# Kernel tuning notes

Measured on AMD Instinct MI355X. Metric: run time of the kernel, lower is better.

The kernel has to match this reference:

```python
import jax, jax.numpy as jnp
import numpy as np

B, NQ, NA, C, L = 8, 2048, 64, 128, 4  # batches, queries/mol, atoms/mol, hidden, num_layers
CUTOFF = 8.0
E_AQ, E_QQ = 131072, 262144


def _ln(x, g, b):
    m = x.mean(-1, keepdims=True)
    v = ((x - m) ** 2).mean(-1, keepdims=True)
    return (x - m) * jax.lax.rsqrt(v + 1e-5) * g + b


def _egnn(p, h_src, h_tgt, pos_src, pos_tgt, t_emb, esrc, etgt):
    (mW1, mb1, mW2, mb2, cW1, cb1, cW2, cb2, nW1, nb1, nW2, nb2, g, b) = p
    rel = pos_tgt[etgt] - pos_src[esrc]                      # (E,3)
    sq = (rel ** 2).sum(-1, keepdims=True)                   # (E,1)
    mi = jnp.concatenate([h_src[esrc], h_tgt[etgt], sq, t_emb[etgt]], -1)  # (E,3C+1)
    msg = jax.nn.silu(jax.nn.silu(mi @ mW1 + mb1) @ mW2 + mb2)             # (E,C)
    w = jnp.tanh(jax.nn.silu(msg @ cW1 + cb1) @ cW2 + cb2)                 # (E,1)
    vel = jnp.zeros_like(pos_tgt).at[etgt].add(w * rel)
    agg = jnp.zeros_like(h_tgt).at[etgt].add(msg)
    u = jnp.concatenate([h_tgt, agg], -1)
    h_new = _ln(h_tgt + (jax.nn.silu(u @ nW1 + nb1) @ nW2 + nb2), g, b)
    return h_new, vel


def setup_inputs() -> dict:
    key = jax.random.key(0)
    ks = iter(jax.random.split(key, 64))
    n = lambda shape, s=0.05: jax.random.normal(next(ks), shape, dtype=jnp.float32) * s
    NQT, NAT = B * NQ, B * NA
    return dict(
        x_t=jax.random.normal(next(ks), (NQT, 3), dtype=jnp.float32) * 3.0,
        t_query=jax.random.uniform(next(ks), (NQT,), dtype=jnp.float32),
        atom_pos=jax.random.normal(next(ks), (NAT, 3), dtype=jnp.float32) * 3.0,
        atom_feat=n((NAT, 256), 1.0),
        edge_aq_src=jax.random.randint(next(ks), (E_AQ,), 0, NAT, dtype=jnp.int32),
        edge_aq_tgt=jax.random.randint(next(ks), (E_AQ,), 0, NQT, dtype=jnp.int32),
        edge_qq_src=jax.random.randint(next(ks), (E_QQ,), 0, NQT, dtype=jnp.int32),
        edge_qq_tgt=jax.random.randint(next(ks), (E_QQ,), 0, NQT, dtype=jnp.int32),
        atom_proj_W=n((256, C)), atom_proj_b=jnp.zeros((C,)),
        time_W1=n((C, 4 * C)), time_b1=jnp.zeros((4 * C,)),
        time_W2=n((4 * C, C)), time_b2=jnp.zeros((C,)),
        qi_W1=n((1, C)), qi_b1=jnp.zeros((C,)),
        qi_W2=n((C, C)), qi_b2=jnp.zeros((C,)),
        msg_W1=n((2 * L, 3 * C + 1, 2 * C)), msg_b1=jnp.zeros((2 * L, 2 * C)),
        msg_W2=n((2 * L, 2 * C, C)), msg_b2=jnp.zeros((2 * L, C)),
        cw_W1=n((2 * L, C, C // 2)), cw_b1=jnp.zeros((2 * L, C // 2)),
        cw_W2=n((2 * L, C // 2, 1)), cw_b2=jnp.zeros((2 * L, 1)),
        nu_W1=n((2 * L, 2 * C, C)), nu_b1=jnp.zeros((2 * L, C)),
        nu_W2=n((2 * L, C, C)), nu_b2=jnp.zeros((2 * L, C)),
        ln_g=jnp.ones((2 * L, C)), ln_b=jnp.zeros((2 * L, C)),
        vo_W1=n((C, C)), vo_b1=jnp.zeros((C,)),
        vo_W2=n((C, 1)), vo_b2=jnp.zeros((1,)),
    )


def reference(x_t, t_query, atom_pos, atom_feat,
              edge_aq_src, edge_aq_tgt, edge_qq_src, edge_qq_tgt,
              atom_proj_W, atom_proj_b,
              time_W1, time_b1, time_W2, time_b2,
              qi_W1, qi_b1, qi_W2, qi_b2,
              msg_W1, msg_b1, msg_W2, msg_b2,
              cw_W1, cw_b1, cw_W2, cw_b2,
              nu_W1, nu_b1, nu_W2, nu_b2,
              ln_g, ln_b,
              vo_W1, vo_b1, vo_W2, vo_b2):
    # atom features (no condition drop: eval mode)
    h_atom = atom_feat @ atom_proj_W + atom_proj_b

    # sinusoidal time embedding per query node
    half = C // 2
    freqs = jnp.exp(-np.log(10000.0) * jnp.arange(half, dtype=jnp.float32) / (half - 1))
    args = t_query[:, None] * freqs[None, :]
    emb = jnp.concatenate([jnp.sin(args), jnp.cos(args)], -1)
    t_emb = jax.nn.silu(emb @ time_W1 + time_b1) @ time_W2 + time_b2

    # init query features: log1p(mean_dist / cutoff), equal-size batches
    q = x_t.reshape(B, NQ, 3)
    a = atom_pos.reshape(B, NA, 3)
    sq = ((q[:, :, None, :] - a[:, None, :, :]) ** 2).sum(-1)  # (B,NQ,NA)
    log_dist = jnp.log1p(jnp.sqrt(sq.mean(-1)) / CUTOFF).reshape(-1, 1)
    h = jax.nn.silu(log_dist @ qi_W1 + qi_b1) @ qi_W2 + qi_b2

    layers = (msg_W1, msg_b1, msg_W2, msg_b2, cw_W1, cw_b1, cw_W2, cw_b2,
              nu_W1, nu_b1, nu_W2, nu_b2, ln_g, ln_b)
    pick = lambda j: tuple(arr[j] for arr in layers)

    vel = jnp.zeros_like(x_t)
    for i in range(L):
        h, dv = _egnn(pick(2 * i), h_atom, h, atom_pos, x_t, t_emb, edge_aq_src, edge_aq_tgt)
        vel = vel + dv
        h, dv = _egnn(pick(2 * i + 1), h, h, x_t, x_t, t_emb, edge_qq_src, edge_qq_tgt)
        vel = vel + dv

    scale = jax.nn.silu(h @ vo_W1 + vo_b1) @ vo_W2 + vo_b2   # (N_q,1)
    return vel * scale
```

## Files before the change

kernel.cpp:

```cpp
#include <hip/hip_runtime.h>

#define NQT 16384
#define NAT 512
#define EAQ 131072
#define EQQ 262144

typedef short short8 __attribute__((ext_vector_type(8)));
typedef float float4v __attribute__((ext_vector_type(4)));

__device__ __forceinline__ float silu_f(float x){ return x / (1.f + __expf(-x)); }

__device__ __forceinline__ short f2bf(float f){
  union { float f; unsigned u; } v; v.f = f;
  unsigned r = v.u + 0x7fff + ((v.u >> 16) & 1);
  return (short)(r >> 16);
}
__device__ __forceinline__ float bf2f(short s){
  union { unsigned u; float f; } v;
  v.u = ((unsigned)(unsigned short)s) << 16;
  return v.f;
}

__global__ __launch_bounds__(256) void k_hist2(
    const int* __restrict__ ta, const int* __restrict__ tq,
    int* __restrict__ ha, int* __restrict__ hq)
{
  int i = blockIdx.x*256 + threadIdx.x;
  atomicAdd(&hq[tq[i]], 1);
  if (i < EAQ) atomicAdd(&ha[ta[i]], 1);
}

__global__ __launch_bounds__(256) void k_scan2(int* __restrict__ ha, int* __restrict__ hq)
{
  int* hist = (blockIdx.x == 0) ? ha : hq;
  __shared__ int part[256];
  int t = threadIdx.x;
  int base = t * 64;
  int s = 0;
  for (int i = 0; i < 64; i++) s += hist[base + i];
  part[t] = s;
  __syncthreads();
  for (int off = 1; off < 256; off <<= 1){
    int v = (t >= off) ? part[t - off] : 0;
    __syncthreads();
    part[t] += v;
    __syncthreads();
  }
  int run = (t == 0) ? 0 : part[t-1];
  for (int i = 0; i < 64; i++){
    int h = hist[base + i];
    hist[base + i] = run;
    run += h;
  }
}

__global__ __launch_bounds__(256) void k_place2(
    const int* __restrict__ sa, const int* __restrict__ ta,
    const int* __restrict__ sq, const int* __restrict__ tq,
    int* __restrict__ ca, int* __restrict__ cq,
    int2* __restrict__ da, int2* __restrict__ dq)
{
  int i = blockIdx.x*256 + threadIdx.x;
  { int tg = tq[i]; int pos = atomicAdd(&cq[tg], 1); dq[pos] = make_int2(sq[i], tg); }
  if (i < EAQ){ int tg = ta[i]; int pos = atomicAdd(&ca[tg], 1); da[pos] = make_int2(sa[i], tg); }
}

__device__ __forceinline__ void pack_one(
    const float* __restrict__ W, short* __restrict__ out,
    int rows, int cols, int ksteps, int ntiles, int idx, int mode)
{
  int l8   = idx & 7;
  int lane = (idx >> 3) & 63;
  int kk   = (idx >> 9) % ksteps;
  int nt   = ((idx >> 9) / ksteps) % ntiles;
  int j    = idx / (512 * ksteps * ntiles);
  int k = kk*32 + (lane >> 4)*8 + l8;
  if (mode == 1) k += (k >= 256);
  else if (mode == 2) k = (k < 128) ? k + 128 : k + 129;
  int n = nt*16 + (lane & 15);
  out[idx] = f2bf(W[(size_t)j*rows*cols + (size_t)k*cols + n]);
}

__global__ __launch_bounds__(256) void k_packall(
    const float* __restrict__ mW1, const float* __restrict__ mW2,
    const float* __restrict__ cW1, const float* __restrict__ nW1,
    const float* __restrict__ nW2, const float* __restrict__ tW1,
    const float* __restrict__ tW2,
    short* W1ap, short* W1bcp, short* W2p, short* W3p,
    short* nW1p, short* nW2p, short* tW1p, short* tW2p)
{
  int b = blockIdx.x, t = threadIdx.x;
  if (b < 1024){ pack_one(mW1, W1ap, 385,256,4,16, b*256+t, 0); return; } b -= 1024;
  if (b < 2048){ pack_one(mW1, W1bcp,385,256,8,16, b*256+t, 2); return; } b -= 2048;
  if (b < 1024){ pack_one(mW2, W2p,  256,128,8, 8, b*256+t, 0); return; } b -= 1024;
  if (b <  256){ pack_one(cW1, W3p,  128, 64,4, 4, b*256+t, 0); return; } b -=  256;
  if (b < 1024){ pack_one(nW1, nW1p, 256,128,8, 8, b*256+t, 0); return; } b -= 1024;
  if (b <  512){ pack_one(nW2, nW2p, 128,128,4, 8, b*256+t, 0); return; } b -=  512;
  if (b <  256){ pack_one(tW1, tW1p, 128,512,4,32, b*256+t, 0); return; } b -=  256;
  pack_one(tW2, tW2p, 512,128,16,8, b*256+t, 0);
}

__global__ __launch_bounds__(256) void k_pre2(
    const float* __restrict__ Xsrc, const float* __restrict__ Xh,
    const float* __restrict__ Xt, const float* __restrict__ biasT,
    const short* __restrict__ WpA, const short* __restrict__ WpB,
    short* __restrict__ Psrc, short* __restrict__ Ptgt, int nblkA)
{
  int t = threadIdx.x;
  int lane = t & 63, w = t >> 6;
  int mrow = lane & 15, quad = lane >> 4;

  if ((int)blockIdx.x < nblkA){
    int m0 = blockIdx.x*64 + w*16;
    short8 areg[4];
    #pragma unroll
    for (int kk = 0; kk < 4; kk++){
      const float* bp = Xsrc + (size_t)(m0+mrow)*128 + kk*32 + quad*8;
      float4 f0 = *(const float4*)(bp);
      float4 f1 = *(const float4*)(bp + 4);
      short8 s;
      s[0]=f2bf(f0.x); s[1]=f2bf(f0.y); s[2]=f2bf(f0.z); s[3]=f2bf(f0.w);
      s[4]=f2bf(f1.x); s[5]=f2bf(f1.y); s[6]=f2bf(f1.z); s[7]=f2bf(f1.w);
      areg[kk] = s;
    }
    #pragma unroll
    for (int nt = 0; nt < 16; nt++){
      float4v acc = {0.f,0.f,0.f,0.f};
      const short8* Bb = (const short8*)(WpA + ((size_t)nt*4)*512 + lane*8);
      #pragma unroll
      for (int kk = 0; kk < 4; kk++)
        acc = __builtin_amdgcn_mfma_f32_16x16x32_bf16(areg[kk], Bb[kk*64], acc, 0, 0, 0);
      #pragma unroll
      for (int r = 0; r < 4; r++)
        Psrc[(size_t)(m0 + quad*4 + r)*256 + nt*16 + mrow] = f2bf(acc[r]);
    }
  } else {
    int m0 = ((int)blockIdx.x - nblkA)*64 + w*16;
    short8 areg[8];
    #pragma unroll
    for (int kk = 0; kk < 8; kk++){
      int k = kk*32 + quad*8;
      const float* bp = (kk >= 4) ? (Xt + (size_t)(m0+mrow)*128 + (k - 128))
                                  : (Xh + (size_t)(m0+mrow)*128 + k);
      float4 f0 = *(const float4*)(bp);
      float4 f1 = *(const float4*)(bp + 4);
      short8 s;
      s[0]=f2bf(f0.x); s[1]=f2bf(f0.y); s[2]=f2bf(f0.z); s[3]=f2bf(f0.w);
      s[4]=f2bf(f1.x); s[5]=f2bf(f1.y); s[6]=f2bf(f1.z); s[7]=f2bf(f1.w);
      areg[kk] = s;
    }
    #pragma unroll
    for (int nt = 0; nt < 16; nt++){
      float4v acc = {0.f,0.f,0.f,0.f};
      const short8* Bb = (const short8*)(WpB + ((size_t)nt*8)*512 + lane*8);
      #pragma unroll
      for (int kk = 0; kk < 8; kk++)
        acc = __builtin_amdgcn_mfma_f32_16x16x32_bf16(areg[kk], Bb[kk*64], acc, 0, 0, 0);
      float bv = biasT[nt*16 + mrow];
      #pragma unroll
      for (int r = 0; r < 4; r++)
        Ptgt[(size_t)(m0 + quad*4 + r)*256 + nt*16 + mrow] = f2bf(acc[r] + bv);
    }
  }
}

__global__ __launch_bounds__(128) void k_hatom(
    const float* __restrict__ feat, const float* __restrict__ W,
    const float* __restrict__ b, float* __restrict__ out)
{
  __shared__ float sf[256];
  int n = blockIdx.x, t = threadIdx.x;
  sf[t]       = feat[n*256 + t];
  sf[t + 128] = feat[n*256 + 128 + t];
  __syncthreads();
  float acc = b[t];
  for (int k = 0; k < 256; k++) acc += sf[k] * W[k*128 + t];
  out[n*128 + t] = acc;
}

__global__ __launch_bounds__(256) void k_temb(
    const float* __restrict__ tq,
    const short* __restrict__ W1p, const float* __restrict__ b1,
    const short* __restrict__ W2p, const float* __restrict__ b2,
    float* __restrict__ temb)
{
  __shared__ __align__(16) short A[32*136];
  __shared__ __align__(16) short B[32*528];
  int t = threadIdx.x;
  int n0 = blockIdx.x * 32;

  {
    int row = t >> 3, l = t & 7;
    float tv = tq[n0 + row];
    short* o = A + row*136;
    #pragma unroll
    for (int i = 0; i < 16; i++){
      int k = l*16 + i;
      int h = k & 63;
      float freq = __expf(-9.210340371976184f * (float)h * (1.f/63.f));
      float a = tv * freq;
      float v = (k < 64) ? __sinf(a) : __cosf(a);
      o[k] = f2bf(v);
    }
  }
  __syncthreads();

  int lane = t & 63, w = t >> 6;
  int mrow = lane & 15, quad = lane >> 4;

  for (int nti = 0; nti < 8; nti++){
    int nt = w*8 + nti;
    #pragma unroll
    for (int mt = 0; mt < 2; mt++){
      float4v acc = {0.f,0.f,0.f,0.f};
      const short8* Ab = (const short8*)(A + (mt*16 + mrow)*136 + quad*8);
      const short8* Bb = (const short8*)(W1p + (size_t)nt*4*512 + lane*8);
      #pragma unroll
      for (int kk = 0; kk < 4; kk++)
        acc = __builtin_amdgcn_mfma_f32_16x16x32_bf16(Ab[kk*4], Bb[kk*64], acc, 0, 0, 0);
      int n = nt*16 + mrow;
      float b1n = b1[n];
      #pragma unroll
      for (int r = 0; r < 4; r++)
        B[(mt*16 + quad*4 + r)*528 + n] = f2bf(silu_f(acc[r] + b1n));
    }
  }
  __syncthreads();

  #pragma unroll
  for (int nti = 0; nti < 2; nti++){
    int nt = w*2 + nti;
    #pragma unroll
    for (int mt = 0; mt < 2; mt++){
      float4v acc = {0.f,0.f,0.f,0.f};
      const short8* Ab = (const short8*)(B + (mt*16 + mrow)*528 + quad*8);
      const short8* Bb = (const short8*)(W2p + (size_t)nt*16*512 + lane*8);
      #pragma unroll
      for (int kk = 0; kk < 16; kk++)
        acc = __builtin_amdgcn_mfma_f32_16x16x32_bf16(Ab[kk*4], Bb[kk*64], acc, 0, 0, 0);
      int n = nt*16 + mrow;
      float b2n = b2[n];
      #pragma unroll
      for (int r = 0; r < 4; r++)
        temb[(size_t)(n0 + mt*16 + quad*4 + r)*128 + n] = acc[r] + b2n;
    }
  }
}

__global__ __launch_bounds__(128) void k_hinit(
    const float* __restrict__ x_t, const float* __restrict__ atom_pos,
    const float* __restrict__ W1, const float* __restrict__ b1,
    const float* __restrict__ W2, const float* __restrict__ b2,
    float* __restrict__ h)
{
  __shared__ float sh[128];
  __shared__ float sld;
  int n = blockIdx.x, t = threadIdx.x;
  float qx = x_t[n*3], qy = x_t[n*3+1], qz = x_t[n*3+2];
  float part = 0.f;
  if (t < 64){
    int a = (n >> 11)*64 + t;
    float dx = qx - atom_pos[a*3];
    float dy = qy - atom_pos[a*3+1];
    float dz = qz - atom_pos[a*3+2];
    part = dx*dx + dy*dy + dz*dz;
  }
  #pragma unroll
  for (int off = 32; off; off >>= 1) part += __shfl_down(part, off);
  if (t == 0) sld = log1pf(sqrtf(part * (1.f/64.f)) * 0.125f);
  __syncthreads();
  float ld = sld;
  sh[t] = silu_f(ld * W1[t] + b1[t]);
  __syncthreads();
  float acc = b2[t];
  for (int k = 0; k < 128; k++) acc += sh[k] * W2[k*128 + t];
  h[(size_t)n*128 + t] = acc;
}

__global__ __launch_bounds__(512, 8) void k_edge(
    const short* __restrict__ Psrc, const short* __restrict__ Ptgt,
    const float* __restrict__ pos_src, const float* __restrict__ pos_tgt,
    const int2* __restrict__ sdesc,
    const float* __restrict__ w1sq,
    const short* __restrict__ W2p, const float* __restrict__ b2,
    const short* __restrict__ W3p, const float* __restrict__ b3,
    const float* __restrict__ W4,  const float* __restrict__ b4,
    float* __restrict__ agg, float* __restrict__ vel)
{
  __shared__ __align__(16) short A2[32*264];
  __shared__ __align__(16) short A3[32*136];
  __shared__ float rel_s[32*3];
  __shared__ int   tgt_s[32];
  float* msgf = (float*)A2;
  float* h3   = (float*)A2;

  int t = threadIdx.x;
  int e0 = blockIdx.x * 32;

  {
    int e = t >> 4, l = t & 15;
    int2 d = sdesc[e0 + e];
    int src = d.x, tgt = d.y;
    float rx = pos_tgt[tgt*3+0] - pos_src[src*3+0];
    float ry = pos_tgt[tgt*3+1] - pos_src[src*3+1];
    float rz = pos_tgt[tgt*3+2] - pos_src[src*3+2];
    float sqv = rx*rx + ry*ry + rz*rz;
    if (l == 0){
      rel_s[e*3+0]=rx; rel_s[e*3+1]=ry; rel_s[e*3+2]=rz;
      tgt_s[e] = tgt;
    }
    const short8* ps = (const short8*)(Psrc + (size_t)src*256);
    const short8* pt = (const short8*)(Ptgt + (size_t)tgt*256);
    #pragma unroll
    for (int c = 0; c < 2; c++){
      int ci = l + 16*c;
      int n0 = ci*8;
      short8 a = ps[ci], b = pt[ci];
      float4 w0 = *(const float4*)(w1sq + n0);
      float4 w1 = *(const float4*)(w1sq + n0 + 4);
      short8 r;
      r[0] = f2bf(silu_f(bf2f(a[0]) + bf2f(b[0]) + sqv*w0.x));
      r[1] = f2bf(silu_f(bf2f(a[1]) + bf2f(b[1]) + sqv*w0.y));
      r[2] = f2bf(silu_f(bf2f(a[2]) + bf2f(b[2]) + sqv*w0.z));
      r[3] = f2bf(silu_f(bf2f(a[3]) + bf2f(b[3]) + sqv*w0.w));
      r[4] = f2bf(silu_f(bf2f(a[4]) + bf2f(b[4]) + sqv*w1.x));
      r[5] = f2bf(silu_f(bf2f(a[5]) + bf2f(b[5]) + sqv*w1.y));
      r[6] = f2bf(silu_f(bf2f(a[6]) + bf2f(b[6]) + sqv*w1.z));
      r[7] = f2bf(silu_f(bf2f(a[7]) + bf2f(b[7]) + sqv*w1.w));
      *(short8*)(A2 + e*264 + n0) = r;
    }
  }
  __syncthreads();

  int lane = t & 63, w = t >> 6;
  int mrow = lane & 15, quad = lane >> 4;

  float4v acc2[2];
  {
    int nt = w;
    #pragma unroll
    for (int mt = 0; mt < 2; mt++){
      float4v acc = {0.f,0.f,0.f,0.f};
      const short8* Ab = (const short8*)(A2 + (mt*16 + mrow)*264 + quad*8);
      const short8* Bb = (const short8*)(W2p + (size_t)nt*8*512 + lane*8);
      #pragma unroll
      for (int kk = 0; kk < 8; kk++)
        acc = __builtin_amdgcn_mfma_f32_16x16x32_bf16(Ab[kk*4], Bb[kk*64], acc, 0, 0, 0);
      acc2[mt] = acc;
    }
  }
  __syncthreads();

  {
    int n = w*16 + mrow;
    float b2n = b2[n];
    #pragma unroll
    for (int mt = 0; mt < 2; mt++){
      #pragma unroll
      for (int r = 0; r < 4; r++){
        int e = mt*16 + quad*4 + r;
        float v = silu_f(acc2[mt][r] + b2n);
        msgf[e*132 + n] = v;
        A3[e*136 + n]   = f2bf(v);
      }
    }
  }
  __syncthreads();

  int nt3 = w & 3, mt3 = w >> 2;
  float4v acc3 = {0.f,0.f,0.f,0.f};
  {
    const short8* Ab = (const short8*)(A3 + (mt3*16 + mrow)*136 + quad*8);
    const short8* Bb = (const short8*)(W3p + (size_t)nt3*4*512 + lane*8);
    #pragma unroll
    for (int kk = 0; kk < 4; kk++)
      acc3 = __builtin_amdgcn_mfma_f32_16x16x32_bf16(Ab[kk*4], Bb[kk*64], acc3, 0, 0, 0);
  }

  {
    int c = t & 127, g = t >> 7;
    int eb = g*8;
    float run = 0.f;
    int cur = tgt_s[eb];
    #pragma unroll
    for (int e = eb; e < eb + 8; e++){
      int tg = tgt_s[e];
      if (tg != cur){
        atomicAdd(&agg[(size_t)cur*128 + c], run);
        run = 0.f; cur = tg;
      }
      run += msgf[e*132 + c];
    }
    atomicAdd(&agg[(size_t)cur*128 + c], run);
  }
  __syncthreads();

  {
    int n = nt3*16 + mrow;
    float b3n = b3[n];
    #pragma unroll
    for (int r = 0; r < 4; r++){
      int e = mt3*16 + quad*4 + r;
      h3[e*68 + n] = silu_f(acc3[r] + b3n);
    }
  }
  __syncthreads();

  {
    int e = t >> 4, l = t & 15;
    float p = 0.f;
    #pragma unroll
    for (int i = 0; i < 4; i++){
      int k = l + 16*i;
      p += h3[e*68 + k] * W4[k];
    }
    p += __shfl_xor(p, 1);
    p += __shfl_xor(p, 2);
    p += __shfl_xor(p, 4);
    p += __shfl_xor(p, 8);
    if (l == 0){
      float wv = tanhf(p + b4[0]);
      int tg = tgt_s[e];
      atomicAdd(&vel[tg*3+0], wv*rel_s[e*3+0]);
      atomicAdd(&vel[tg*3+1], wv*rel_s[e*3+1]);
      atomicAdd(&vel[tg*3+2], wv*rel_s[e*3+2]);
    }
  }
}

__global__ __launch_bounds__(256) void k_node(
    const float* __restrict__ h, float* __restrict__ agg,
    const short* __restrict__ W1p, const float* __restrict__ b1,
    const short* __restrict__ W2p, const float* __restrict__ b2,
    const float* __restrict__ g, const float* __restrict__ bb_,
    float* __restrict__ h_out)
{
  __shared__ __align__(16) short A[32*264];
  __shared__ __align__(16) short B[32*136];
  float* r = (float*)A;
  int t = threadIdx.x;
  int n0 = blockIdx.x * 32;

  {
    int row = t >> 3, l = t & 7;
    const float4* hr = (const float4*)(h + (size_t)(n0+row)*128);
    float4*       ar = (float4*)(agg + (size_t)(n0+row)*128);
    short* o = A + row*264;
    float4 z = make_float4(0.f,0.f,0.f,0.f);
    #pragma unroll
    for (int i = 0; i < 4; i++){
      int k4 = l + 8*i;
      float4 a = hr[k4];
      o[k4*4+0]=f2bf(a.x); o[k4*4+1]=f2bf(a.y); o[k4*4+2]=f2bf(a.z); o[k4*4+3]=f2bf(a.w);
      float4 b = ar[k4];
      o[128 + k4*4+0]=f2bf(b.x); o[128 + k4*4+1]=f2bf(b.y);
      o[128 + k4*4+2]=f2bf(b.z); o[128 + k4*4+3]=f2bf(b.w);
      ar[k4] = z;
    }
  }
  __syncthreads();

  int lane = t & 63, w = t >> 6;
  int mrow = lane & 15, quad = lane >> 4;

  float4v accA[2][2];
  #pragma unroll
  for (int nti = 0; nti < 2; nti++){
    int nt = w*2 + nti;
    #pragma unroll
    for (int mt = 0; mt < 2; mt++){
      float4v acc = {0.f,0.f,0.f,0.f};
      const short8* Ab = (const short8*)(A + (mt*16 + mrow)*264 + quad*8);
      const short8* Bb = (const short8*)(W1p + (size_t)nt*8*512 + lane*8);
      #pragma unroll
      for (int kk = 0; kk < 8; kk++)
        acc = __builtin_amdgcn_mfma_f32_16x16x32_bf16(Ab[kk*4], Bb[kk*64], acc, 0, 0, 0);
      accA[nti][mt] = acc;
    }
  }
  __syncthreads();

  #pragma unroll
  for (int nti = 0; nti < 2; nti++){
    int n = (w*2 + nti)*16 + mrow;
    float b1n = b1[n];
    #pragma unroll
    for (int mt = 0; mt < 2; mt++){
      #pragma unroll
      for (int rr = 0; rr < 4; rr++){
        int e = mt*16 + quad*4 + rr;
        B[e*136 + n] = f2bf(silu_f(accA[nti][mt][rr] + b1n));
      }
    }
  }
  __syncthreads();

  #pragma unroll
  for (int nti = 0; nti < 2; nti++){
    int nt = w*2 + nti;
    #pragma unroll
    for (int mt = 0; mt < 2; mt++){
      float4v acc = {0.f,0.f,0.f,0.f};
      const short8* Ab = (const short8*)(B + (mt*16 + mrow)*136 + quad*8);
      const short8* Bb = (const short8*)(W2p + (size_t)nt*4*512 + lane*8);
      #pragma unroll
      for (int kk = 0; kk < 4; kk++)
        acc = __builtin_amdgcn_mfma_f32_16x16x32_bf16(Ab[kk*4], Bb[kk*64], acc, 0, 0, 0);
      int n = nt*16 + mrow;
      float b2n = b2[n];
      #pragma unroll
      for (int rr = 0; rr < 4; rr++){
        int e = mt*16 + quad*4 + rr;
        r[e*132 + n] = h[(size_t)(n0+e)*128 + n] + acc[rr] + b2n;
      }
    }
  }
  __syncthreads();

  {
    int lane2 = t & 63, wid = t >> 6;
    #pragma unroll
    for (int nn = 0; nn < 8; nn++){
      int row = wid*8 + nn;
      float a = r[row*132 + lane2], bv = r[row*132 + lane2 + 64];
      float s = a + bv, ss = a*a + bv*bv;
      #pragma unroll
      for (int off = 1; off < 64; off <<= 1){
        s  += __shfl_xor(s, off);
        ss += __shfl_xor(ss, off);
      }
      float mean = s * (1.f/128.f);
      float var  = ss * (1.f/128.f) - mean*mean;
      float rstd = rsqrtf(var + 1e-5f);
      float* ho = h_out + (size_t)(n0+row)*128;
      ho[lane2]      = (a  - mean)*rstd*g[lane2]      + bb_[lane2];
      ho[lane2 + 64] = (bv - mean)*rstd*g[lane2 + 64] + bb_[lane2 + 64];
    }
  }
}

__global__ __launch_bounds__(128) void k_out(
    const float* __restrict__ h, const float* __restrict__ vel,
    const float* __restrict__ W1, const float* __restrict__ b1,
    const float* __restrict__ W2, const float* __restrict__ b2,
    float* __restrict__ out)
{
  __shared__ float sh[128];
  __shared__ float spart[2];
  int n = blockIdx.x, t = threadIdx.x;
  sh[t] = h[(size_t)n*128 + t];
  __syncthreads();
  float acc = b1[t];
  for (int k = 0; k < 128; k++) acc += sh[k] * W1[k*128 + t];
  float p = silu_f(acc) * W2[t];
  #pragma unroll
  for (int off = 32; off; off >>= 1) p += __shfl_down(p, off);
  if ((t & 63) == 0) spart[t >> 6] = p;
  __syncthreads();
  if (t < 3){
    float scale = spart[0] + spart[1] + b2[0];
    out[n*3 + t] = vel[n*3 + t] * scale;
  }
}

extern "C" void kernel_launch(void* const* d_in, const int* in_sizes, int n_in,
                              void* d_out, int out_size, void* d_ws, size_t ws_size,
                              hipStream_t stream)
{
  const float* x_t       = (const float*)d_in[0];
  const float* t_query   = (const float*)d_in[1];
  const float* atom_pos  = (const float*)d_in[2];
  const float* atom_feat = (const float*)d_in[3];
  const int*   e_aq_s = (const int*)d_in[4];
  const int*   e_aq_t = (const int*)d_in[5];
  const int*   e_qq_s = (const int*)d_in[6];
  const int*   e_qq_t = (const int*)d_in[7];
  const float* apW  = (const float*)d_in[8];
  const float* apb  = (const float*)d_in[9];
  const float* tW1  = (const float*)d_in[10];
  const float* tb1  = (const float*)d_in[11];
  const float* tW2  = (const float*)d_in[12];
  const float* tb2  = (const float*)d_in[13];
  const float* qiW1 = (const float*)d_in[14];
  const float* qib1 = (const float*)d_in[15];
  const float* qiW2 = (const float*)d_in[16];
  const float* qib2 = (const float*)d_in[17];
  const float* mW1  = (const float*)d_in[18];
  const float* mb1  = (const float*)d_in[19];
  const float* mW2  = (const float*)d_in[20];
  const float* mb2  = (const float*)d_in[21];
  const float* cW1  = (const float*)d_in[22];
  const float* cb1  = (const float*)d_in[23];
  const float* cW2  = (const float*)d_in[24];
  const float* cb2  = (const float*)d_in[25];
  const float* nW1  = (const float*)d_in[26];
  const float* nb1  = (const float*)d_in[27];
  const float* nW2  = (const float*)d_in[28];
  const float* nb2  = (const float*)d_in[29];
  const float* lng  = (const float*)d_in[30];
  const float* lnb  = (const float*)d_in[31];
  const float* voW1 = (const float*)d_in[32];
  const float* vob1 = (const float*)d_in[33];
  const float* voW2 = (const float*)d_in[34];
  const float* vob2 = (const float*)d_in[35];
  float* out = (float*)d_out;

  float* ws     = (float*)d_ws;
  float* h_atom = ws;
  float* temb   = h_atom + 65536;
  float* hA     = temb + 2097152;
  float* hB     = hA + 2097152;
  float* agg    = hB + 2097152;
  float* vel    = agg + 2097152;
  short* W1ap   = (short*)(vel + 49152);
  short* W1bcp  = W1ap + 262144;
  short* W2p    = W1bcp + 524288;
  short* W3p    = W2p + 262144;
  short* nW1p   = W3p + 65536;
  short* nW2p   = nW1p + 262144;
  short* tW1p   = nW2p + 131072;
  short* tW2p   = tW1p + 65536;
  short* Psrc   = tW2p + 65536;
  short* Ptgt   = Psrc + 4194304;
  int*   hist_a = (int*)(Ptgt + 4194304);
  int*   hist_q = hist_a + 16384;
  int2*  desc_a = (int2*)(hist_q + 16384);
  int2*  desc_q = desc_a + EAQ;

  hipMemsetAsync(hist_a, 0, 2*16384*sizeof(int), stream);
  k_hist2<<<EQQ/256, 256, 0, stream>>>(e_aq_t, e_qq_t, hist_a, hist_q);
  k_scan2<<<2, 256, 0, stream>>>(hist_a, hist_q);
  k_place2<<<EQQ/256, 256, 0, stream>>>(e_aq_s, e_aq_t, e_qq_s, e_qq_t,
                                        hist_a, hist_q, desc_a, desc_q);

  k_packall<<<6400, 256, 0, stream>>>(mW1, mW2, cW1, nW1, nW2, tW1, tW2,
      W1ap, W1bcp, W2p, W3p, nW1p, nW2p, tW1p, tW2p);

  hipMemsetAsync(agg, 0, (size_t)(NQT*128 + NQT*3)*sizeof(float), stream);
  k_hatom<<<NAT, 128, 0, stream>>>(atom_feat, apW, apb, h_atom);
  k_temb<<<NQT/32, 256, 0, stream>>>(t_query, tW1p, tb1, tW2p, tb2, temb);
  k_hinit<<<NQT, 128, 0, stream>>>(x_t, atom_pos, qiW1, qib1, qiW2, qib2, hA);

  float* hc = hA; float* hn = hB;
  for (int i = 0; i < 4; i++){
    for (int half = 0; half < 2; half++){
      int j = 2*i + half;
      const int2* dsc = half ? desc_q : desc_a;
      int E = half ? EQQ : EAQ;
      const float* hsrc = half ? hc : h_atom;
      int nblkA = (half ? NQT : NAT) / 64;

      k_pre2<<<nblkA + NQT/64, 256, 0, stream>>>(hsrc, hc, temb,
          mb1 + (size_t)j*256,
          W1ap + (size_t)j*32768, W1bcp + (size_t)j*65536,
          Psrc, Ptgt, nblkA);

      k_edge<<<E/32, 512, 0, stream>>>(Psrc, Ptgt,
          half ? x_t : atom_pos, x_t, dsc,
          mW1 + (size_t)j*385*256 + 65536,
          W2p + (size_t)j*32768, mb2 + (size_t)j*128,
          W3p + (size_t)j*8192,  cb1 + (size_t)j*64,
          cW2 + (size_t)j*64,    cb2 + (size_t)j,
          agg, vel);
      k_node<<<NQT/32, 256, 0, stream>>>(hc, agg,
          nW1p + (size_t)j*32768, nb1 + (size_t)j*128,
          nW2p + (size_t)j*16384, nb2 + (size_t)j*128,
          lng + (size_t)j*128,    lnb + (size_t)j*128, hn);
      float* tmp = hc; hc = hn; hn = tmp;
    }
  }
  k_out<<<NQT, 128, 0, stream>>>(hc, vel, voW1, vob1, voW2, vob2, out);
}
```

Before: 1.541 ms.

## Fuse next-layer message projections into node update and shrink edge blocks

Removes the per-layer k_pre2 launch. The atom-source projections for all four atom-to-query layers are precomputed once in a new k_pre0 kernel. The target and query-source projections for the next layer are computed inside k_node from the freshly normalized h, kept in LDS, so h is not re-read from global memory. k_edge moves from 512 to 256 threads per block, with each thread doing twice the work, and the launch_bounds occupancy hint is dropped. The cost is more LDS and work per k_node block and possibly lower parallelism in k_edge.

```diff
diff --git a/kernel.cpp b/kernel.cpp
--- a/kernel.cpp
+++ b/kernel.cpp
@@ -100,22 +100,25 @@
   pack_one(tW2, tW2p, 512,128,16,8, b*256+t, 0);
 }
 
-__global__ __launch_bounds__(256) void k_pre2(
-    const float* __restrict__ Xsrc, const float* __restrict__ Xh,
-    const float* __restrict__ Xt, const float* __restrict__ biasT,
-    const short* __restrict__ WpA, const short* __restrict__ WpB,
-    short* __restrict__ Psrc, short* __restrict__ Ptgt, int nblkA)
+__global__ __launch_bounds__(256) void k_pre0(
+    const float* __restrict__ hA, const float* __restrict__ temb,
+    const float* __restrict__ mb1_0, const short* __restrict__ W1bcp0,
+    const float* __restrict__ h_atom, const short* __restrict__ W1ap_base,
+    short* __restrict__ Ptgt, short* __restrict__ psrc_aq)
 {
   int t = threadIdx.x;
   int lane = t & 63, w = t >> 6;
   int mrow = lane & 15, quad = lane >> 4;
-
-  if ((int)blockIdx.x < nblkA){
-    int m0 = blockIdx.x*64 + w*16;
-    short8 areg[4];
-    #pragma unroll
-    for (int kk = 0; kk < 4; kk++){
-      const float* bp = Xsrc + (size_t)(m0+mrow)*128 + kk*32 + quad*8;
+  int b = blockIdx.x;
+
+  if (b < NQT/64){
+    int m0 = b*64 + w*16;
+    short8 areg[8];
+    #pragma unroll
+    for (int kk = 0; kk < 8; kk++){
+      int k = kk*32 + quad*8;
+      const float* bp = (kk >= 4) ? (temb + (size_t)(m0+mrow)*128 + (k - 128))
+                                  : (hA   + (size_t)(m0+mrow)*128 + k);
       float4 f0 = *(const float4*)(bp);
       float4 f1 = *(const float4*)(bp + 4);
       short8 s;
@@ -126,22 +129,24 @@
     #pragma unroll
     for (int nt = 0; nt < 16; nt++){
       float4v acc = {0.f,0.f,0.f,0.f};
-      const short8* Bb = (const short8*)(WpA + ((size_t)nt*4)*512 + lane*8);
-      #pragma unroll
-      for (int kk = 0; kk < 4; kk++)
+      const short8* Bb = (const short8*)(W1bcp0 + ((size_t)nt*8)*512 + lane*8);
+      #pragma unroll
+      for (int kk = 0; kk < 8; kk++)
         acc = __builtin_amdgcn_mfma_f32_16x16x32_bf16(areg[kk], Bb[kk*64], acc, 0, 0, 0);
+      float bv = mb1_0[nt*16 + mrow];
       #pragma unroll
       for (int r = 0; r < 4; r++)
-        Psrc[(size_t)(m0 + quad*4 + r)*256 + nt*16 + mrow] = f2bf(acc[r]);
+        Ptgt[(size_t)(m0 + quad*4 + r)*256 + nt*16 + mrow] = f2bf(acc[r] + bv);
     }
   } else {
-    int m0 = ((int)blockIdx.x - nblkA)*64 + w*16;
-    short8 areg[8];
-    #pragma unroll
-    for (int kk = 0; kk < 8; kk++){
-      int k = kk*32 + quad*8;
-      const float* bp = (kk >= 4) ? (Xt + (size_t)(m0+mrow)*128 + (k - 128))
-                                  : (Xh + (size_t)(m0+mrow)*128 + k);
+    int bb = b - NQT/64;
+    int idx = bb >> 3;
+    int m0 = (bb & 7)*64 + w*16;
+    const short* Wp = W1ap_base + (size_t)(2*idx)*32768;
+    short8 areg[4];
+    #pragma unroll
+    for (int kk = 0; kk < 4; kk++){
+      const float* bp = h_atom + (size_t)(m0+mrow)*128 + kk*32 + quad*8;
       float4 f0 = *(const float4*)(bp);
       float4 f1 = *(const float4*)(bp + 4);
       short8 s;
@@ -152,14 +157,13 @@
     #pragma unroll
     for (int nt = 0; nt < 16; nt++){
       float4v acc = {0.f,0.f,0.f,0.f};
-      const short8* Bb = (const short8*)(WpB + ((size_t)nt*8)*512 + lane*8);
-      #pragma unroll
-      for (int kk = 0; kk < 8; kk++)
+      const short8* Bb = (const short8*)(Wp + ((size_t)nt*4)*512 + lane*8);
+      #pragma unroll
+      for (int kk = 0; kk < 4; kk++)
         acc = __builtin_amdgcn_mfma_f32_16x16x32_bf16(areg[kk], Bb[kk*64], acc, 0, 0, 0);
-      float bv = biasT[nt*16 + mrow];
       #pragma unroll
       for (int r = 0; r < 4; r++)
-        Ptgt[(size_t)(m0 + quad*4 + r)*256 + nt*16 + mrow] = f2bf(acc[r] + bv);
+        psrc_aq[(size_t)idx*131072 + (size_t)(m0 + quad*4 + r)*256 + nt*16 + mrow] = f2bf(acc[r]);
     }
   }
 }
@@ -277,7 +281,7 @@
   h[(size_t)n*128 + t] = acc;
 }
 
-__global__ __launch_bounds__(512, 8) void k_edge(
+__global__ __launch_bounds__(256) void k_edge(
     const short* __restrict__ Psrc, const short* __restrict__ Ptgt,
     const float* __restrict__ pos_src, const float* __restrict__ pos_tgt,
     const int2* __restrict__ sdesc,
@@ -298,7 +302,7 @@
   int e0 = blockIdx.x * 32;
 
   {
-    int e = t >> 4, l = t & 15;
+    int e = t >> 3, l = t & 7;
     int2 d = sdesc[e0 + e];
     int src = d.x, tgt = d.y;
     float rx = pos_tgt[tgt*3+0] - pos_src[src*3+0];
@@ -312,8 +316,8 @@
     const short8* ps = (const short8*)(Psrc + (size_t)src*256);
     const short8* pt = (const short8*)(Ptgt + (size_t)tgt*256);
     #pragma unroll
-    for (int c = 0; c < 2; c++){
-      int ci = l + 16*c;
+    for (int c = 0; c < 4; c++){
+      int ci = c*8 + l;
       int n0 = ci*8;
       short8 a = ps[ci], b = pt[ci];
       float4 w0 = *(const float4*)(w1sq + n0);
@@ -335,9 +339,10 @@
   int lane = t & 63, w = t >> 6;
   int mrow = lane & 15, quad = lane >> 4;
 
-  float4v acc2[2];
-  {
-    int nt = w;
+  float4v acc2[2][2];
+  #pragma unroll
+  for (int nti = 0; nti < 2; nti++){
+    int nt = w*2 + nti;
     #pragma unroll
     for (int mt = 0; mt < 2; mt++){
       float4v acc = {0.f,0.f,0.f,0.f};
@@ -346,20 +351,21 @@
       #pragma unroll
       for (int kk = 0; kk < 8; kk++)
         acc = __builtin_amdgcn_mfma_f32_16x16x32_bf16(Ab[kk*4], Bb[kk*64], acc, 0, 0, 0);
-      acc2[mt] = acc;
-    }
-  }
-  __syncthreads();
-
-  {
-    int n = w*16 + mrow;
+      acc2[nti][mt] = acc;
+    }
+  }
+  __syncthreads();
+
+  #pragma unroll
+  for (int nti = 0; nti < 2; nti++){
+    int n = (w*2 + nti)*16 + mrow;
     float b2n = b2[n];
     #pragma unroll
     for (int mt = 0; mt < 2; mt++){
       #pragma unroll
       for (int r = 0; r < 4; r++){
         int e = mt*16 + quad*4 + r;
-        float v = silu_f(acc2[mt][r] + b2n);
+        float v = silu_f(acc2[nti][mt][r] + b2n);
         msgf[e*132 + n] = v;
         A3[e*136 + n]   = f2bf(v);
       }
@@ -367,23 +373,27 @@
   }
   __syncthreads();
 
-  int nt3 = w & 3, mt3 = w >> 2;
-  float4v acc3 = {0.f,0.f,0.f,0.f};
+  float4v acc3[2];
   {
-    const short8* Ab = (const short8*)(A3 + (mt3*16 + mrow)*136 + quad*8);
-    const short8* Bb = (const short8*)(W3p + (size_t)nt3*4*512 + lane*8);
-    #pragma unroll
-    for (int kk = 0; kk < 4; kk++)
-      acc3 = __builtin_amdgcn_mfma_f32_16x16x32_bf16(Ab[kk*4], Bb[kk*64], acc3, 0, 0, 0);
+    int nt = w;
+    #pragma unroll
+    for (int mt = 0; mt < 2; mt++){
+      float4v acc = {0.f,0.f,0.f,0.f};
+      const short8* Ab = (const short8*)(A3 + (mt*16 + mrow)*136 + quad*8);
+      const short8* Bb = (const short8*)(W3p + (size_t)nt*4*512 + lane*8);
+      #pragma unroll
+      for (int kk = 0; kk < 4; kk++)
+        acc = __builtin_amdgcn_mfma_f32_16x16x32_bf16(Ab[kk*4], Bb[kk*64], acc, 0, 0, 0);
+      acc3[mt] = acc;
+    }
   }
 
   {
-    int c = t & 127, g = t >> 7;
-    int eb = g*8;
+    int c = t & 127, hh = t >> 7;
+    int eb = hh*16;
     float run = 0.f;
     int cur = tgt_s[eb];
-    #pragma unroll
-    for (int e = eb; e < eb + 8; e++){
+    for (int e = eb; e < eb + 16; e++){
       int tg = tgt_s[e];
       if (tg != cur){
         atomicAdd(&agg[(size_t)cur*128 + c], run);
@@ -396,28 +406,30 @@
   __syncthreads();
 
   {
-    int n = nt3*16 + mrow;
+    int n = w*16 + mrow;
     float b3n = b3[n];
     #pragma unroll
-    for (int r = 0; r < 4; r++){
-      int e = mt3*16 + quad*4 + r;
-      h3[e*68 + n] = silu_f(acc3[r] + b3n);
+    for (int mt = 0; mt < 2; mt++){
+      #pragma unroll
+      for (int r = 0; r < 4; r++){
+        int e = mt*16 + quad*4 + r;
+        h3[e*68 + n] = silu_f(acc3[mt][r] + b3n);
+      }
     }
   }
   __syncthreads();
 
   {
-    int e = t >> 4, l = t & 15;
+    int e = t >> 3, l = t & 7;
     float p = 0.f;
     #pragma unroll
-    for (int i = 0; i < 4; i++){
-      int k = l + 16*i;
+    for (int i = 0; i < 8; i++){
+      int k = l + 8*i;
       p += h3[e*68 + k] * W4[k];
     }
     p += __shfl_xor(p, 1);
     p += __shfl_xor(p, 2);
     p += __shfl_xor(p, 4);
-    p += __shfl_xor(p, 8);
     if (l == 0){
       float wv = tanhf(p + b4[0]);
       int tg = tgt_s[e];
@@ -433,10 +445,16 @@
     const short* __restrict__ W1p, const float* __restrict__ b1,
     const short* __restrict__ W2p, const float* __restrict__ b2,
     const float* __restrict__ g, const float* __restrict__ bb_,
-    float* __restrict__ h_out)
+    float* __restrict__ h_out,
+    int produce,
+    const float* __restrict__ temb,
+    const short* __restrict__ W1bcN, const float* __restrict__ mb1N,
+    const short* __restrict__ W1aN,
+    short* __restrict__ Ptgt, short* __restrict__ PsrcQ)
 {
   __shared__ __align__(16) short A[32*264];
   __shared__ __align__(16) short B[32*136];
+  __shared__ __align__(16) short S[32*264];
   float* r = (float*)A;
   int t = threadIdx.x;
   int n0 = blockIdx.x * 32;
@@ -445,7 +463,9 @@
     int row = t >> 3, l = t & 7;
     const float4* hr = (const float4*)(h + (size_t)(n0+row)*128);
     float4*       ar = (float4*)(agg + (size_t)(n0+row)*128);
+    const float4* te = (const float4*)(temb + (size_t)(n0+row)*128);
     short* o = A + row*264;
+    short* so = S + row*264 + 128;
     float4 z = make_float4(0.f,0.f,0.f,0.f);
     #pragma unroll
     for (int i = 0; i < 4; i++){
@@ -456,6 +476,11 @@
       o[128 + k4*4+0]=f2bf(b.x); o[128 + k4*4+1]=f2bf(b.y);
       o[128 + k4*4+2]=f2bf(b.z); o[128 + k4*4+3]=f2bf(b.w);
       ar[k4] = z;
+      if (produce){
+        float4 c = te[k4];
+        so[k4*4+0]=f2bf(c.x); so[k4*4+1]=f2bf(c.y);
+        so[k4*4+2]=f2bf(c.z); so[k4*4+3]=f2bf(c.w);
+      }
     }
   }
   __syncthreads();
@@ -532,9 +557,54 @@
       float mean = s * (1.f/128.f);
       float var  = ss * (1.f/128.f) - mean*mean;
       float rstd = rsqrtf(var + 1e-5f);
+      float v0 = (a  - mean)*rstd*g[lane2]      + bb_[lane2];
+      float v1 = (bv - mean)*rstd*g[lane2 + 64] + bb_[lane2 + 64];
       float* ho = h_out + (size_t)(n0+row)*128;
-      ho[lane2]      = (a  - mean)*rstd*g[lane2]      + bb_[lane2];
-      ho[lane2 + 64] = (bv - mean)*rstd*g[lane2 + 64] + bb_[lane2 + 64];
+      ho[lane2]      = v0;
+      ho[lane2 + 64] = v1;
+      S[row*264 + lane2]      = f2bf(v0);
+      S[row*264 + lane2 + 64] = f2bf(v1);
+    }
+  }
+  if (!produce) return;
+  __syncthreads();
+
+  #pragma unroll
+  for (int nti = 0; nti < 4; nti++){
+    int nt = w*4 + nti;
+    #pragma unroll
+    for (int mt = 0; mt < 2; mt++){
+      float4v acc = {0.f,0.f,0.f,0.f};
+      const short8* Ab = (const short8*)(S + (mt*16 + mrow)*264 + quad*8);
+      const short8* Bb = (const short8*)(W1bcN + (size_t)nt*8*512 + lane*8);
+      #pragma unroll
+      for (int kk = 0; kk < 8; kk++)
+        acc = __builtin_amdgcn_mfma_f32_16x16x32_bf16(Ab[kk*4], Bb[kk*64], acc, 0, 0, 0);
+      int n = nt*16 + mrow;
+      float bv = mb1N[n];
+      #pragma unroll
+      for (int rr = 0; rr < 4; rr++)
+        Ptgt[(size_t)(n0 + mt*16 + quad*4 + rr)*256 + n] = f2bf(acc[rr] + bv);
+    }
+  }
+
+  if (produce == 2){
+    #pragma unroll
+    for (int nti = 0; nti < 4; nti++){
+      int nt = w*4 + nti;
+      #pragma unroll
+      for (int mt = 0; mt < 2; mt++){
+        float4v acc = {0.f,0.f,0.f,0.f};
+        const short8* Ab = (const short8*)(S + (mt*16 + mrow)*264 + quad*8);
+        const short8* Bb = (const short8*)(W1aN + (size_t)nt*4*512 + lane*8);
+        #pragma unroll
+        for (int kk = 0; kk < 4; kk++)
+          acc = __builtin_amdgcn_mfma_f32_16x16x32_bf16(Ab[kk*4], Bb[kk*64], acc, 0, 0, 0);
+        int n = nt*16 + mrow;
+        #pragma unroll
+        for (int rr = 0; rr < 4; rr++)
+          PsrcQ[(size_t)(n0 + mt*16 + quad*4 + rr)*256 + n] = f2bf(acc[rr]);
+      }
     }
   }
 }
@@ -620,9 +690,10 @@
   short* nW2p   = nW1p + 262144;
   short* tW1p   = nW2p + 131072;
   short* tW2p   = tW1p + 65536;
-  short* Psrc   = tW2p + 65536;
-  short* Ptgt   = Psrc + 4194304;
-  int*   hist_a = (int*)(Ptgt + 4194304);
+  short* PsrcQ  = tW2p + 65536;
+  short* Ptgt   = PsrcQ + 4194304;
+  short* psrc_aq= Ptgt + 4194304;
+  int*   hist_a = (int*)(psrc_aq + 524288);
   int*   hist_q = hist_a + 16384;
   int2*  desc_a = (int2*)(hist_q + 16384);
   int2*  desc_q = desc_a + EAQ;
@@ -641,33 +712,35 @@
   k_temb<<<NQT/32, 256, 0, stream>>>(t_query, tW1p, tb1, tW2p, tb2, temb);
   k_hinit<<<NQT, 128, 0, stream>>>(x_t, atom_pos, qiW1, qib1, qiW2, qib2, hA);
 
+  k_pre0<<<NQT/64 + 32, 256, 0, stream>>>(hA, temb, mb1, W1bcp, h_atom, W1ap,
+                                          Ptgt, psrc_aq);
+
   float* hc = hA; float* hn = hB;
-  for (int i = 0; i < 4; i++){
-    for (int half = 0; half < 2; half++){
-      int j = 2*i + half;
-      const int2* dsc = half ? desc_q : desc_a;
-      int E = half ? EQQ : EAQ;
-      const float* hsrc = half ? hc : h_atom;
-      int nblkA = (half ? NQT : NAT) / 64;
-
-      k_pre2<<<nblkA + NQT/64, 256, 0, stream>>>(hsrc, hc, temb,
-          mb1 + (size_t)j*256,
-          W1ap + (size_t)j*32768, W1bcp + (size_t)j*65536,
-          Psrc, Ptgt, nblkA);
-
-      k_edge<<<E/32, 512, 0, stream>>>(Psrc, Ptgt,
-          half ? x_t : atom_pos, x_t, dsc,
-          mW1 + (size_t)j*385*256 + 65536,
-          W2p + (size_t)j*32768, mb2 + (size_t)j*128,
-          W3p + (size_t)j*8192,  cb1 + (size_t)j*64,
-          cW2 + (size_t)j*64,    cb2 + (size_t)j,
-          agg, vel);
-      k_node<<<NQT/32, 256, 0, stream>>>(hc, agg,
-          nW1p + (size_t)j*32768, nb1 + (size_t)j*128,
-          nW2p + (size_t)j*16384, nb2 + (size_t)j*128,
-          lng + (size_t)j*128,    lnb + (size_t)j*128, hn);
-      float* tmp = hc; hc = hn; hn = tmp;
-    }
+  for (int j = 0; j < 8; j++){
+    int half = j & 1;
+    const int2* dsc = half ? desc_q : desc_a;
+    int E = half ? EQQ : EAQ;
+    const short* psrc = half ? PsrcQ : (psrc_aq + (size_t)(j >> 1)*131072);
+
+    k_edge<<<E/32, 256, 0, stream>>>(psrc, Ptgt,
+        half ? x_t : atom_pos, x_t, dsc,
+        mW1 + (size_t)j*385*256 + 65536,
+        W2p + (size_t)j*32768, mb2 + (size_t)j*128,
+        W3p + (size_t)j*8192,  cb1 + (size_t)j*64,
+        cW2 + (size_t)j*64,    cb2 + (size_t)j,
+        agg, vel);
+
+    int jn = (j < 7) ? (j + 1) : 7;
+    int produce = (j == 7) ? 0 : ((half == 0) ? 2 : 1);
+    k_node<<<NQT/32, 256, 0, stream>>>(hc, agg,
+        nW1p + (size_t)j*32768, nb1 + (size_t)j*128,
+        nW2p + (size_t)j*16384, nb2 + (size_t)j*128,
+        lng + (size_t)j*128,    lnb + (size_t)j*128, hn,
+        produce, temb,
+        W1bcp + (size_t)jn*65536, mb1 + (size_t)jn*256,
+        W1ap + (size_t)jn*32768,
+        Ptgt, PsrcQ);
+    float* tmp = hc; hc = hn; hn = tmp;
   }
   k_out<<<NQT, 128, 0, stream>>>(hc, vel, voW1, vob1, voW2, vob2, out);
 }
```

After: 1.318 ms. -14.5%, faster.
